# Kernel tuning notes

Measured on AMD Instinct MI355X. Metric: run time of the kernel, lower is better.

The kernel has to match this reference:

```python
import jax, jax.numpy as jnp
import numpy as np

B, D = 4096, 512
STEPS = 50
LR, B1, B2, EPS = 0.01, 0.9, 0.999, 1e-8  # torch.optim.Adam defaults with lr=0.01


def setup_inputs() -> dict:
    key = jax.random.key(0)
    k1, k2, k3, k4 = jax.random.split(key, 4)
    s = jax.random.normal(k1, (B, D), dtype=jnp.float32)
    target_confidence = jax.random.uniform(k2, (B, 1), dtype=jnp.float32)
    # nn.Linear(style_dim, 1) init: U(-1/sqrt(D), 1/sqrt(D))
    lim = 1.0 / np.sqrt(D)
    W = jax.random.uniform(k3, (1, D), dtype=jnp.float32, minval=-lim, maxval=lim)
    b = jax.random.uniform(k4, (1,), dtype=jnp.float32, minval=-lim, maxval=lim)
    return {"s": s, "target_confidence": target_confidence, "W": W, "b": b}


def reference(s, target_confidence, W, b):
    # loss(x) = mse(sigmoid(x W^T + b), t) + l1(x, s); grad taken w.r.t. x only.
    def loss_fn(x):
        p = jax.nn.sigmoid(x @ W.T + b)                      # [B, 1]
        mse = jnp.mean((p - target_confidence) ** 2)
        d = x - s
        # stop_gradient(sign) so d|d|/dx = sign(d), with sign(0) = 0 (matches torch l1_loss subgradient)
        l1 = jnp.mean(jax.lax.stop_gradient(jnp.sign(d)) * d)
        return mse + l1

    grad_fn = jax.grad(loss_fn)

    def adam_step(carry, _):
        x, m, v, t = carry
        g = grad_fn(x)
        t = t + 1.0
        m = B1 * m + (1.0 - B1) * g
        v = B2 * v + (1.0 - B2) * g * g
        m_hat = m / (1.0 - B1 ** t)
        v_hat = v / (1.0 - B2 ** t)
        x = x - LR * m_hat / (jnp.sqrt(v_hat) + EPS)
        return (x, m, v, t), None

    init = (s, jnp.zeros_like(s), jnp.zeros_like(s), jnp.float32(0.0))
    (adjusted_s, _, _, _), _ = jax.lax.scan(adam_step, init, None, length=STEPS)
    return adjusted_s
```

## Files before the change

### kernel.cpp

```cpp
#include <hip/hip_runtime.h>

#define B_ 4096
#define D_ 512
#define STEPS_ 50

#define DPP_ADD(x, ctrl) \
    ((x) + __int_as_float(__builtin_amdgcn_update_dpp( \
        0, __float_as_int(x), (ctrl), 0xf, 0xf, true)))

__device__ __forceinline__ float wave64_sum(float x) {
    x = DPP_ADD(x, 0x111);
    x = DPP_ADD(x, 0x112);
    x = DPP_ADD(x, 0x114);
    x = DPP_ADD(x, 0x118);
    x = DPP_ADD(x, 0x142);
    x = DPP_ADD(x, 0x143);
    return __int_as_float(__builtin_amdgcn_readlane(__float_as_int(x), 63));
}

__device__ __forceinline__ float coef_from_z(float z, float t) {
    const float e = __expf(-z);
    const float q = __builtin_amdgcn_rcpf(1.0f + e);
    return (q - t) * (e * (q * q));
}

__global__ __launch_bounds__(64, 1) void adam_rows_kernel(
    const float* __restrict__ s,
    const float* __restrict__ tgt,
    const float* __restrict__ W,
    const float* __restrict__ bias_p,
    float* __restrict__ out)
{
    const int lane = threadIdx.x;
    const int rb = blockIdx.x * 4;

    float vAn;
    {
        const float t1 = (float)(lane + 1);
        const float p1 = exp2f(t1 * -0.15200309344505f);
        const float p2 = exp2f(t1 * -0.00144345345258f);
        vAn = (-0.0316227766017f * __builtin_amdgcn_sqrtf(1.0f - p2)) *
              __builtin_amdgcn_rcpf(1.0f - p1);
    }

    const float4* W4 = (const float4*)W;
    const float4 wa = W4[lane], wb = W4[lane + 64];
    const float b = bias_p[0];

    const float c_mse = 0x1p-11f;
    const float K     = 2048.0f;
    const float c_l1  = 0x1p-21f;

    float ws[8] = {wa.x * c_mse, wa.y * c_mse, wa.z * c_mse, wa.w * c_mse,
                   wb.x * c_mse, wb.y * c_mse, wb.z * c_mse, wb.w * c_mse};

    float M[4][8], V[4][8], dl[4][8];
    float du[4], zb[4], tg[4], c[4];

#pragma unroll
    for (int r = 0; r < 4; ++r) {
        const float4* sr = (const float4*)(s + (size_t)(rb + r) * D_);
        const float4 sa = sr[lane], sb = sr[lane + 64];
        tg[r] = tgt[rb + r];
        const float e[8] = {sa.x, sa.y, sa.z, sa.w, sb.x, sb.y, sb.z, sb.w};
        float za = 0.0f;
#pragma unroll
        for (int k = 0; k < 8; ++k) za = fmaf(e[k], ws[k], za);
        zb[r] = fmaf(K, wave64_sum(za), b);
    }

    {
        const float An0 =
            __int_as_float(__builtin_amdgcn_readlane(__float_as_int(vAn), 0));
#pragma unroll
        for (int r = 0; r < 4; ++r) {
            const float cr = coef_from_z(zb[r], tg[r]);
            float a = 0.0f;
#pragma unroll
            for (int k = 0; k < 8; ++k) {
                const float g = cr * ws[k];
                M[r][k] = g;
                V[r][k] = fmaf(g, g, 1e-30f);
                dl[r][k] = (An0 * g) * __builtin_amdgcn_rsqf(V[r][k]);
                a = fmaf(dl[r][k], ws[k], a);
            }
            du[r] = a;
        }
    }

    c[0] = coef_from_z(fmaf(K, wave64_sum(du[0]), zb[0]), tg[0]);
    c[1] = coef_from_z(fmaf(K, wave64_sum(du[1]), zb[1]), tg[1]);
    c[2] = coef_from_z(fmaf(K, wave64_sum(du[2]), zb[2]), tg[2]);

#pragma unroll 1
    for (int step = 1; step < STEPS_; ++step) {
        const float An =
            __int_as_float(__builtin_amdgcn_readlane(__float_as_int(vAn), step));

        c[3] = coef_from_z(fmaf(K, wave64_sum(du[3]), zb[3]), tg[3]);

#pragma unroll
        for (int r = 0; r < 4; ++r) {
            float a = 0.0f;
#pragma unroll
            for (int k = 0; k < 8; ++k) {
                const float g =
                    fmaf(c[r], ws[k], __builtin_copysignf(c_l1, dl[r][k]));
                M[r][k] = fmaf(0.9f,   M[r][k], g);
                V[r][k] = fmaf(0.999f, V[r][k], g * g);
                dl[r][k] =
                    fmaf(An * M[r][k], __builtin_amdgcn_rsqf(V[r][k]), dl[r][k]);
                a = fmaf(dl[r][k], ws[k], a);
            }
            du[r] = a;
            if (r != 3)
                c[r] = coef_from_z(fmaf(K, wave64_sum(a), zb[r]), tg[r]);
        }
    }

#pragma unroll
    for (int r = 0; r < 4; ++r) {
        const float4* sr = (const float4*)(s + (size_t)(rb + r) * D_);
        const float4 sa = sr[lane], sb = sr[lane + 64];
        float4 oa = {sa.x + dl[r][0], sa.y + dl[r][1],
                     sa.z + dl[r][2], sa.w + dl[r][3]};
        float4 ob = {sb.x + dl[r][4], sb.y + dl[r][5],
                     sb.z + dl[r][6], sb.w + dl[r][7]};
        float4* orow = (float4*)(out + (size_t)(rb + r) * D_);
        orow[lane]      = oa;
        orow[lane + 64] = ob;
    }
}

extern "C" void kernel_launch(void* const* d_in, const int* in_sizes, int n_in,
                              void* d_out, int out_size, void* d_ws, size_t ws_size,
                              hipStream_t stream) {
    const float* s    = (const float*)d_in[0];
    const float* tgt  = (const float*)d_in[1];
    const float* W    = (const float*)d_in[2];
    const float* bias = (const float*)d_in[3];
    float* out = (float*)d_out;

    adam_rows_kernel<<<dim3(B_ / 4), dim3(64), 0, stream>>>(s, tgt, W, bias, out);
}
```

Before: 92.50 us.

## Map one row per 16-lane group instead of four rows per full wave

Each 64-lane wave now handles its four rows with one 16-lane group per row, each lane holding 32 elements, instead of every lane holding 8 elements of all four rows. The per-step dot-product reduction shrinks to a 16-lane row DPP sum plus a ds_bpermute broadcast, replacing four serialized wave-wide reductions with readlane. This removes the staggered per-row dependency chain and cross-row reduction latency. The cost is a longer per-lane element loop, more registers per lane, and an LDS-path permute on the critical chain of every step.

```diff
diff --git a/kernel.cpp b/kernel.cpp
--- a/kernel.cpp
+++ b/kernel.cpp
@@ -8,14 +8,16 @@
     ((x) + __int_as_float(__builtin_amdgcn_update_dpp( \
         0, __float_as_int(x), (ctrl), 0xf, 0xf, true)))
 
-__device__ __forceinline__ float wave64_sum(float x) {
+__device__ __forceinline__ float row16_sum(float x) {
     x = DPP_ADD(x, 0x111);
     x = DPP_ADD(x, 0x112);
     x = DPP_ADD(x, 0x114);
     x = DPP_ADD(x, 0x118);
-    x = DPP_ADD(x, 0x142);
-    x = DPP_ADD(x, 0x143);
-    return __int_as_float(__builtin_amdgcn_readlane(__float_as_int(x), 63));
+    return x;
+}
+
+__device__ __forceinline__ float grp_bcast15(float x, int vsel) {
+    return __int_as_float(__builtin_amdgcn_ds_bpermute(vsel, __float_as_int(x)));
 }
 
 __device__ __forceinline__ float coef_from_z(float z, float t) {
@@ -32,7 +34,10 @@
     float* __restrict__ out)
 {
     const int lane = threadIdx.x;
-    const int rb = blockIdx.x * 4;
+    const int grp  = lane >> 4;
+    const int j    = lane & 15;
+    const int row  = blockIdx.x * 4 + grp;
+    const int vsel = ((lane & 48) | 15) << 2;
 
     float vAn;
     {
@@ -43,92 +48,83 @@
               __builtin_amdgcn_rcpf(1.0f - p1);
     }
 
-    const float4* W4 = (const float4*)W;
-    const float4 wa = W4[lane], wb = W4[lane + 64];
-    const float b = bias_p[0];
-
     const float c_mse = 0x1p-11f;
     const float K     = 2048.0f;
     const float c_l1  = 0x1p-21f;
 
-    float ws[8] = {wa.x * c_mse, wa.y * c_mse, wa.z * c_mse, wa.w * c_mse,
-                   wb.x * c_mse, wb.y * c_mse, wb.z * c_mse, wb.w * c_mse};
+    const float4* W4  = (const float4*)W;
+    const float4* sr4 = (const float4*)(s + (size_t)row * D_);
 
-    float M[4][8], V[4][8], dl[4][8];
-    float du[4], zb[4], tg[4], c[4];
+    float ws[32], dl[32], M[32], V[32];
+#pragma unroll
+    for (int q = 0; q < 8; ++q) {
+        const float4 w = W4[j + 16 * q];
+        ws[4*q+0] = w.x * c_mse; ws[4*q+1] = w.y * c_mse;
+        ws[4*q+2] = w.z * c_mse; ws[4*q+3] = w.w * c_mse;
+    }
 
+    float vzb;
+    {
+        float a0 = 0.0f, a1 = 0.0f, a2 = 0.0f, a3 = 0.0f;
 #pragma unroll
-    for (int r = 0; r < 4; ++r) {
-        const float4* sr = (const float4*)(s + (size_t)(rb + r) * D_);
-        const float4 sa = sr[lane], sb = sr[lane + 64];
-        tg[r] = tgt[rb + r];
-        const float e[8] = {sa.x, sa.y, sa.z, sa.w, sb.x, sb.y, sb.z, sb.w};
-        float za = 0.0f;
-#pragma unroll
-        for (int k = 0; k < 8; ++k) za = fmaf(e[k], ws[k], za);
-        zb[r] = fmaf(K, wave64_sum(za), b);
+        for (int q = 0; q < 8; ++q) {
+            const float4 e = sr4[j + 16 * q];
+            a0 = fmaf(e.x, ws[4*q+0], a0);
+            a1 = fmaf(e.y, ws[4*q+1], a1);
+            a2 = fmaf(e.z, ws[4*q+2], a2);
+            a3 = fmaf(e.w, ws[4*q+3], a3);
+        }
+        vzb = fmaf(K, row16_sum((a0 + a1) + (a2 + a3)), bias_p[0]);
     }
+    const float vtg = tgt[row];
+
+    float vc;
 
     {
         const float An0 =
             __int_as_float(__builtin_amdgcn_readlane(__float_as_int(vAn), 0));
+        vc = grp_bcast15(coef_from_z(vzb, vtg), vsel);
+        float a0 = 0.0f, a1 = 0.0f, a2 = 0.0f, a3 = 0.0f;
 #pragma unroll
-        for (int r = 0; r < 4; ++r) {
-            const float cr = coef_from_z(zb[r], tg[r]);
-            float a = 0.0f;
-#pragma unroll
-            for (int k = 0; k < 8; ++k) {
-                const float g = cr * ws[k];
-                M[r][k] = g;
-                V[r][k] = fmaf(g, g, 1e-30f);
-                dl[r][k] = (An0 * g) * __builtin_amdgcn_rsqf(V[r][k]);
-                a = fmaf(dl[r][k], ws[k], a);
-            }
-            du[r] = a;
+        for (int k = 0; k < 32; ++k) {
+            const float g = vc * ws[k];
+            M[k] = g;
+            V[k] = fmaf(g, g, 1e-30f);
+            dl[k] = (An0 * g) * __builtin_amdgcn_rsqf(V[k]);
+            float* acc = (k & 2) ? ((k & 1) ? &a3 : &a2) : ((k & 1) ? &a1 : &a0);
+            *acc = fmaf(dl[k], ws[k], *acc);
         }
+        const float vz = fmaf(K, row16_sum((a0 + a1) + (a2 + a3)), vzb);
+        vc = grp_bcast15(coef_from_z(vz, vtg), vsel);
     }
-
-    c[0] = coef_from_z(fmaf(K, wave64_sum(du[0]), zb[0]), tg[0]);
-    c[1] = coef_from_z(fmaf(K, wave64_sum(du[1]), zb[1]), tg[1]);
-    c[2] = coef_from_z(fmaf(K, wave64_sum(du[2]), zb[2]), tg[2]);
 
 #pragma unroll 1
     for (int step = 1; step < STEPS_; ++step) {
         const float An =
             __int_as_float(__builtin_amdgcn_readlane(__float_as_int(vAn), step));
-
-        c[3] = coef_from_z(fmaf(K, wave64_sum(du[3]), zb[3]), tg[3]);
-
+        float a0 = 0.0f, a1 = 0.0f, a2 = 0.0f, a3 = 0.0f;
 #pragma unroll
-        for (int r = 0; r < 4; ++r) {
-            float a = 0.0f;
-#pragma unroll
-            for (int k = 0; k < 8; ++k) {
-                const float g =
-                    fmaf(c[r], ws[k], __builtin_copysignf(c_l1, dl[r][k]));
-                M[r][k] = fmaf(0.9f,   M[r][k], g);
-                V[r][k] = fmaf(0.999f, V[r][k], g * g);
-                dl[r][k] =
-                    fmaf(An * M[r][k], __builtin_amdgcn_rsqf(V[r][k]), dl[r][k]);
-                a = fmaf(dl[r][k], ws[k], a);
-            }
-            du[r] = a;
-            if (r != 3)
-                c[r] = coef_from_z(fmaf(K, wave64_sum(a), zb[r]), tg[r]);
+        for (int k = 0; k < 32; ++k) {
+            const float g = fmaf(vc, ws[k], __builtin_copysignf(c_l1, dl[k]));
+            M[k] = fmaf(0.9f,   M[k], g);
+            V[k] = fmaf(0.999f, V[k], g * g);
+            dl[k] = fmaf(An * M[k], __builtin_amdgcn_rsqf(V[k]), dl[k]);
+            float* acc = (k & 2) ? ((k & 1) ? &a3 : &a2) : ((k & 1) ? &a1 : &a0);
+            *acc = fmaf(dl[k], ws[k], *acc);
+        }
+        if (step != STEPS_ - 1) {
+            const float vz = fmaf(K, row16_sum((a0 + a1) + (a2 + a3)), vzb);
+            vc = grp_bcast15(coef_from_z(vz, vtg), vsel);
         }
     }
 
+    float4* orow = (float4*)(out + (size_t)row * D_);
 #pragma unroll
-    for (int r = 0; r < 4; ++r) {
-        const float4* sr = (const float4*)(s + (size_t)(rb + r) * D_);
-        const float4 sa = sr[lane], sb = sr[lane + 64];
-        float4 oa = {sa.x + dl[r][0], sa.y + dl[r][1],
-                     sa.z + dl[r][2], sa.w + dl[r][3]};
-        float4 ob = {sb.x + dl[r][4], sb.y + dl[r][5],
-                     sb.z + dl[r][6], sb.w + dl[r][7]};
-        float4* orow = (float4*)(out + (size_t)(rb + r) * D_);
-        orow[lane]      = oa;
-        orow[lane + 64] = ob;
+    for (int q = 0; q < 8; ++q) {
+        const float4 e = sr4[j + 16 * q];
+        float4 o = {e.x + dl[4*q+0], e.y + dl[4*q+1],
+                    e.z + dl[4*q+2], e.w + dl[4*q+3]};
+        orow[j + 16 * q] = o;
     }
 }
 
```

Measured after the change: 91.27 us. Within noise of the previous version (-1.3%).

## Process one row per wave instead of four interleaved rows

Applied to the files above, without the earlier changes.

Each 64-lane block now handles a single row, launching four times as many blocks and allowing several waves per SIMD. Latency from the per-step wave reduction and exp is meant to be hidden by hardware wave interleaving rather than manual software pipelining across four rows. This cuts register pressure but repeats W loads and setup per row, and relies on the scheduler to overlap the serial chains.

```diff
diff --git a/kernel.cpp b/kernel.cpp
--- a/kernel.cpp
+++ b/kernel.cpp
@@ -24,7 +24,7 @@
     return (q - t) * (e * (q * q));
 }
 
-__global__ __launch_bounds__(64, 1) void adam_rows_kernel(
+__global__ __launch_bounds__(64, 4) void adam_rows_kernel(
     const float* __restrict__ s,
     const float* __restrict__ tgt,
     const float* __restrict__ W,
@@ -32,7 +32,7 @@
     float* __restrict__ out)
 {
     const int lane = threadIdx.x;
-    const int rb = blockIdx.x * 4;
+    const int row  = blockIdx.x;
 
     float vAn;
     {
@@ -43,90 +43,72 @@
               __builtin_amdgcn_rcpf(1.0f - p1);
     }
 
-    const float4* W4 = (const float4*)W;
-    const float4 wa = W4[lane], wb = W4[lane + 64];
-    const float b = bias_p[0];
-
     const float c_mse = 0x1p-11f;
     const float K     = 2048.0f;
     const float c_l1  = 0x1p-21f;
 
+    const float4* W4  = (const float4*)W;
+    const float4* sr4 = (const float4*)(s + (size_t)row * D_);
+
+    const float4 wa = W4[lane], wb = W4[lane + 64];
     float ws[8] = {wa.x * c_mse, wa.y * c_mse, wa.z * c_mse, wa.w * c_mse,
                    wb.x * c_mse, wb.y * c_mse, wb.z * c_mse, wb.w * c_mse};
 
-    float M[4][8], V[4][8], dl[4][8];
-    float du[4], zb[4], tg[4], c[4];
+    float dl[8], M[8], V[8];
 
-#pragma unroll
-    for (int r = 0; r < 4; ++r) {
-        const float4* sr = (const float4*)(s + (size_t)(rb + r) * D_);
-        const float4 sa = sr[lane], sb = sr[lane + 64];
-        tg[r] = tgt[rb + r];
+    float zb;
+    {
+        const float4 sa = sr4[lane], sb = sr4[lane + 64];
         const float e[8] = {sa.x, sa.y, sa.z, sa.w, sb.x, sb.y, sb.z, sb.w};
         float za = 0.0f;
 #pragma unroll
         for (int k = 0; k < 8; ++k) za = fmaf(e[k], ws[k], za);
-        zb[r] = fmaf(K, wave64_sum(za), b);
+        zb = fmaf(K, wave64_sum(za), bias_p[0]);
     }
+    const float tg = tgt[row];
+
+    float du;
 
     {
+        const float c0 = coef_from_z(zb, tg);
         const float An0 =
             __int_as_float(__builtin_amdgcn_readlane(__float_as_int(vAn), 0));
+        float a = 0.0f;
 #pragma unroll
-        for (int r = 0; r < 4; ++r) {
-            const float cr = coef_from_z(zb[r], tg[r]);
-            float a = 0.0f;
-#pragma unroll
-            for (int k = 0; k < 8; ++k) {
-                const float g = cr * ws[k];
-                M[r][k] = g;
-                V[r][k] = fmaf(g, g, 1e-30f);
-                dl[r][k] = (An0 * g) * __builtin_amdgcn_rsqf(V[r][k]);
-                a = fmaf(dl[r][k], ws[k], a);
-            }
-            du[r] = a;
+        for (int k = 0; k < 8; ++k) {
+            const float g = c0 * ws[k];
+            M[k] = g;
+            V[k] = fmaf(g, g, 1e-30f);
+            dl[k] = (An0 * g) * __builtin_amdgcn_rsqf(V[k]);
+            a = fmaf(dl[k], ws[k], a);
         }
+        du = a;
     }
-
-    c[0] = coef_from_z(fmaf(K, wave64_sum(du[0]), zb[0]), tg[0]);
-    c[1] = coef_from_z(fmaf(K, wave64_sum(du[1]), zb[1]), tg[1]);
-    c[2] = coef_from_z(fmaf(K, wave64_sum(du[2]), zb[2]), tg[2]);
 
 #pragma unroll 1
     for (int step = 1; step < STEPS_; ++step) {
         const float An =
             __int_as_float(__builtin_amdgcn_readlane(__float_as_int(vAn), step));
+        const float c =
+            coef_from_z(fmaf(K, wave64_sum(du), zb), tg);
 
-        c[3] = coef_from_z(fmaf(K, wave64_sum(du[3]), zb[3]), tg[3]);
-
+        float a = 0.0f;
 #pragma unroll
-        for (int r = 0; r < 4; ++r) {
-            float a = 0.0f;
-#pragma unroll
-            for (int k = 0; k < 8; ++k) {
-                const float g =
-                    fmaf(c[r], ws[k], __builtin_copysignf(c_l1, dl[r][k]));
-                M[r][k] = fmaf(0.9f,   M[r][k], g);
-                V[r][k] = fmaf(0.999f, V[r][k], g * g);
-                dl[r][k] =
-                    fmaf(An * M[r][k], __builtin_amdgcn_rsqf(V[r][k]), dl[r][k]);
-                a = fmaf(dl[r][k], ws[k], a);
-            }
-            du[r] = a;
-            if (r != 3)
-                c[r] = coef_from_z(fmaf(K, wave64_sum(a), zb[r]), tg[r]);
+        for (int k = 0; k < 8; ++k) {
+            const float g = fmaf(c, ws[k], __builtin_copysignf(c_l1, dl[k]));
+            M[k] = fmaf(0.9f,   M[k], g);
+            V[k] = fmaf(0.999f, V[k], g * g);
+            dl[k] = fmaf(An * M[k], __builtin_amdgcn_rsqf(V[k]), dl[k]);
+            a = fmaf(dl[k], ws[k], a);
         }
+        du = a;
     }
 
-#pragma unroll
-    for (int r = 0; r < 4; ++r) {
-        const float4* sr = (const float4*)(s + (size_t)(rb + r) * D_);
-        const float4 sa = sr[lane], sb = sr[lane + 64];
-        float4 oa = {sa.x + dl[r][0], sa.y + dl[r][1],
-                     sa.z + dl[r][2], sa.w + dl[r][3]};
-        float4 ob = {sb.x + dl[r][4], sb.y + dl[r][5],
-                     sb.z + dl[r][6], sb.w + dl[r][7]};
-        float4* orow = (float4*)(out + (size_t)(rb + r) * D_);
+    {
+        const float4 sa = sr4[lane], sb = sr4[lane + 64];
+        float4 oa = {sa.x + dl[0], sa.y + dl[1], sa.z + dl[2], sa.w + dl[3]};
+        float4 ob = {sb.x + dl[4], sb.y + dl[5], sb.z + dl[6], sb.w + dl[7]};
+        float4* orow = (float4*)(out + (size_t)row * D_);
         orow[lane]      = oa;
         orow[lane + 64] = ob;
     }
@@ -141,5 +123,5 @@
     const float* bias = (const float*)d_in[3];
     float* out = (float*)d_out;
 
-    adam_rows_kernel<<<dim3(B_ / 4), dim3(64), 0, stream>>>(s, tgt, W, bias, out);
+    adam_rows_kernel<<<dim3(B_), dim3(64), 0, stream>>>(s, tgt, W, bias, out);
 }
```

After: 92.24 us. No clear change (-0.3%).
